# Kernel tuning notes

Hardware: AMD Instinct MI355X
Metric: run time of the kernel (lower is better)

Reference implementation:

```python
import jax, jax.numpy as jnp
import numpy as np

D = 32      # input_size
H = 256     # hidden_size
B = 4096    # batch
EPS = 1e-12

def _masks(order="A"):
    # Standard MADE degree-based masks. order 'A' = natural ordering.
    deg_in = np.arange(1, D + 1) if order == "A" else np.arange(D, 0, -1)
    deg_h = (np.arange(H) % (D - 1)) + 1
    m0 = (deg_h[None, :] >= deg_in[:, None]).astype(np.float32)  # [D,H] input->hidden
    m1 = (deg_h[None, :] >= deg_h[:, None]).astype(np.float32)   # [H,H] hidden->hidden
    m2 = (deg_in[None, :] > deg_h[:, None]).astype(np.float32)   # [H,D] hidden->output (strict)
    return jnp.asarray(m0), jnp.asarray(m1), jnp.asarray(m2)

M0, M1, M2 = _masks()

def _made(y, W0, b0, W1, b1, W2, b2):
    # masked MLP: D -> H -> H -> D (num_hiddens=2 hidden layers)
    h = jax.nn.relu(y @ (W0 * M0) + b0)
    h = jax.nn.relu(h @ (W1 * M1) + b1)
    return h @ (W2 * M2) + b2

def setup_inputs() -> dict:
    key = jax.random.key(0)
    ks = jax.random.split(key, 8)
    def w(k, fi, fo):
        return jax.random.normal(k, (fi, fo), jnp.float32) / np.sqrt(fi)
    inp = {"x": jax.random.normal(ks[0], (B, D), jnp.float32)}
    i = 1
    for n in ("mu", "lv"):
        inp[n + "_W0"] = w(ks[i], D, H); inp[n + "_b0"] = jnp.zeros((H,), jnp.float32); i += 1
        inp[n + "_W1"] = w(ks[i], H, H); inp[n + "_b1"] = jnp.zeros((H,), jnp.float32); i += 1
        inp[n + "_W2"] = w(ks[i], H, D); inp[n + "_b2"] = jnp.zeros((D,), jnp.float32); i += 1
    return inp

def reference(x, mu_W0, mu_b0, mu_W1, mu_b1, mu_W2, mu_b2,
              lv_W0, lv_b0, lv_W1, lv_b1, lv_W2, lv_b2):
    # AFMADEBlock.forward: D sequential fixed-point iterations of the
    def step(carry, _):
        y, _ls = carry
        mu = _made(y, mu_W0, mu_b0, mu_W1, mu_b1, mu_W2, mu_b2)
        logstd = _made(y, lv_W0, lv_b0, lv_W1, lv_b1, lv_W2, lv_b2) * 0.5
        y_new = (x - mu) / (jnp.exp(logstd) + EPS)
        return (y_new, logstd), None
    init = (jnp.zeros_like(x), jnp.zeros_like(x))
    (y, logstd), _ = jax.lax.scan(step, init, None, length=D)
    return y, logstd.sum(axis=1)
```

## Files before the change

### kernel.cpp

```cpp
#include <hip/hip_runtime.h>

#define DD   32
#define HH   256
#define BB   4096
#define RR   2
#define EPSF 1e-12f

__device__ __forceinline__ int made_pi(int p) {
    return (p < 72) ? (p / 9) + 31 * (p % 9)
                    : (8 + (p - 72) / 8) + 31 * ((p - 72) % 8);
}
__device__ __forceinline__ int made_off(int d) {
    return (d <= 9) ? 9 * (d - 1) : 8 * d;
}

#define NW0   (DD * HH)
#define NW1   (HH * HH)
#define NW2   (DD * HH)
#define NETF  (NW0 + NW1 + NW2 + HH + HH)
#define WSNEED ((size_t)(2 * NETF) * 4)

__global__ void made_prep(
    const float* __restrict__ muW0, const float* __restrict__ mub0,
    const float* __restrict__ muW1, const float* __restrict__ mub1,
    const float* __restrict__ muW2,
    const float* __restrict__ lvW0, const float* __restrict__ lvb0,
    const float* __restrict__ lvW1, const float* __restrict__ lvb1,
    const float* __restrict__ lvW2,
    float* __restrict__ ws)
{
    const int t = threadIdx.x;
    const int b = blockIdx.x;
    __shared__ float rowbuf[HH];

    if (b < 512) {
        const int n = b >> 8, p = b & 255;
        const int h = made_pi(p);
        const float* W1 = n ? lvW1 : muW1;
        float* o = ws + (size_t)n * NETF;
        *reinterpret_cast<float4*>(&rowbuf[4 * t]) =
            *reinterpret_cast<const float4*>(W1 + h * HH + 4 * t);
        __syncthreads();
        float4 w;
        w.x = rowbuf[made_pi(4 * t + 0)];
        w.y = rowbuf[made_pi(4 * t + 1)];
        w.z = rowbuf[made_pi(4 * t + 2)];
        w.w = rowbuf[made_pi(4 * t + 3)];
        *reinterpret_cast<float4*>(o + NW0 + p * HH + 4 * t) = w;
        if (t == 0) {
            o[NW0 + NW1 + NW2 + p]      = (n ? lvb0 : mub0)[h];
            o[NW0 + NW1 + NW2 + HH + p] = (n ? lvb1 : mub1)[h];
        }
    } else {
        const int idx   = b - 512;
        const int n     = idx >> 6;
        const int which = (idx >> 5) & 1;
        const int i     = idx & 31;
        float* o = ws + (size_t)n * NETF;
        if (which == 0) {
            const float* W0 = n ? lvW0 : muW0;
            *reinterpret_cast<float4*>(&rowbuf[4 * t]) =
                *reinterpret_cast<const float4*>(W0 + i * HH + 4 * t);
            __syncthreads();
            float4 w;
            w.x = rowbuf[made_pi(4 * t + 0)];
            w.y = rowbuf[made_pi(4 * t + 1)];
            w.z = rowbuf[made_pi(4 * t + 2)];
            w.w = rowbuf[made_pi(4 * t + 3)];
            *reinterpret_cast<float4*>(o + i * HH + 4 * t) = w;
        } else {
            const float* W2 = n ? lvW2 : muW2;
            float4 w;
            w.x = W2[made_pi(4 * t + 0) * DD + i];
            w.y = W2[made_pi(4 * t + 1) * DD + i];
            w.z = W2[made_pi(4 * t + 2) * DD + i];
            w.w = W2[made_pi(4 * t + 3) * DD + i];
            *reinterpret_cast<float4*>(o + NW0 + NW1 + i * HH + 4 * t) = w;
        }
    }
}

__global__ __launch_bounds__(256, 2) void made_main(
    const float* __restrict__ ws, const float* __restrict__ x,
    const float* __restrict__ mub2, const float* __restrict__ lvb2,
    float* __restrict__ out)
{
    const int lane = threadIdx.x & 63;
    const int wv   = threadIdx.x >> 6;
    const int row0 = ((blockIdx.x << 2) + wv) * RR;
    const int c4   = lane << 2;

    const float* W0p[2] = {ws,             ws + NETF};
    const float* W1p[2] = {ws + NW0,       ws + NETF + NW0};
    const float* W2p[2] = {ws + NW0 + NW1, ws + NETF + NW0 + NW1};

    float h0[2][4][RR], h1[2][4][RR], r1[2][4][RR];
    #pragma unroll
    for (int n = 0; n < 2; ++n) {
        const float* bb = ws + (size_t)n * NETF + NW0 + NW1 + NW2;
        const float4 v0 = *reinterpret_cast<const float4*>(bb + c4);
        const float4 v1 = *reinterpret_cast<const float4*>(bb + HH + c4);
        const float a0[4] = {v0.x, v0.y, v0.z, v0.w};
        const float a1[4] = {v1.x, v1.y, v1.z, v1.w};
        #pragma unroll
        for (int s = 0; s < 4; ++s)
            #pragma unroll
            for (int r = 0; r < RR; ++r) {
                h0[n][s][r] = a0[s];
                h1[n][s][r] = a1[s];
                r1[n][s][r] = 0.f;
            }
    }

    __shared__ float A[4][2][RR][12];

    float yprev[RR], lsum[RR], ysave[RR];
    #pragma unroll
    for (int r = 0; r < RR; ++r) { yprev[r] = 0.f; lsum[r] = 0.f; ysave[r] = 0.f; }

    for (int d = 0; d < DD; ++d) {
        const int off  = (d >= 1) ? made_off(d) : 0;
        const int off2 = made_off(d + 1);
        const int nk   = off2 - off;

        if (d >= 1) {
            const int ls = off >> 2;
            if (lane >= ls) {
                #pragma unroll
                for (int n = 0; n < 2; ++n) {
                    const float4 w = *reinterpret_cast<const float4*>(
                        W0p[n] + (d - 1) * HH + c4);
                    #pragma unroll
                    for (int r = 0; r < RR; ++r) {
                        h0[n][0][r] = fmaf(yprev[r], w.x, h0[n][0][r]);
                        h0[n][1][r] = fmaf(yprev[r], w.y, h0[n][1][r]);
                        h0[n][2][r] = fmaf(yprev[r], w.z, h0[n][2][r]);
                        h0[n][3][r] = fmaf(yprev[r], w.w, h0[n][3][r]);
                    }
                }
            }
            #pragma unroll
            for (int s = 0; s < 4; ++s) {
                const int p = c4 + s;
                if (p >= off && p < off2) {
                    const int k = p - off;
                    #pragma unroll
                    for (int r = 0; r < RR; ++r) {
                        A[wv][0][r][k] = fmaxf(h0[0][s][r], 0.f);
                        A[wv][1][r][k] = fmaxf(h0[1][s][r], 0.f);
                    }
                }
            }
            float av[2][RR][9];
            #pragma unroll
            for (int n = 0; n < 2; ++n)
                #pragma unroll
                for (int r = 0; r < RR; ++r) {
                    const float4 a03 = *reinterpret_cast<const float4*>(&A[wv][n][r][0]);
                    const float4 a47 = *reinterpret_cast<const float4*>(&A[wv][n][r][4]);
                    av[n][r][0] = a03.x; av[n][r][1] = a03.y;
                    av[n][r][2] = a03.z; av[n][r][3] = a03.w;
                    av[n][r][4] = a47.x; av[n][r][5] = a47.y;
                    av[n][r][6] = a47.z; av[n][r][7] = a47.w;
                    av[n][r][8] = A[wv][n][r][8];
                }

            if (lane >= ls) {
                #pragma unroll
                for (int n = 0; n < 2; ++n) {
                    const float* W1r = W1p[n] + off * HH + c4;
                    #pragma unroll
                    for (int k = 0; k < 8; ++k) {
                        const float4 w = *reinterpret_cast<const float4*>(W1r + k * HH);
                        #pragma unroll
                        for (int r = 0; r < RR; ++r) {
                            h1[n][0][r] = fmaf(av[n][r][k], w.x, h1[n][0][r]);
                            h1[n][1][r] = fmaf(av[n][r][k], w.y, h1[n][1][r]);
                            h1[n][2][r] = fmaf(av[n][r][k], w.z, h1[n][2][r]);
                            h1[n][3][r] = fmaf(av[n][r][k], w.w, h1[n][3][r]);
                        }
                    }
                }
                if (nk == 9) {
                    #pragma unroll
                    for (int n = 0; n < 2; ++n) {
                        const float4 w = *reinterpret_cast<const float4*>(
                            W1p[n] + (off + 8) * HH + c4);
                        #pragma unroll
                        for (int r = 0; r < RR; ++r) {
                            h1[n][0][r] = fmaf(av[n][r][8], w.x, h1[n][0][r]);
                            h1[n][1][r] = fmaf(av[n][r][8], w.y, h1[n][1][r]);
                            h1[n][2][r] = fmaf(av[n][r][8], w.z, h1[n][2][r]);
                            h1[n][3][r] = fmaf(av[n][r][8], w.w, h1[n][3][r]);
                        }
                    }
                }
            }
            #pragma unroll
            for (int s = 0; s < 4; ++s) {
                const int p = c4 + s;
                if (p >= off && p < off2) {
                    #pragma unroll
                    for (int r = 0; r < RR; ++r) {
                        r1[0][s][r] = fmaxf(h1[0][s][r], 0.f);
                        r1[1][s][r] = fmaxf(h1[1][s][r], 0.f);
                    }
                }
            }
        }

        float red[2][RR];
        #pragma unroll
        for (int n = 0; n < 2; ++n)
            #pragma unroll
            for (int r = 0; r < RR; ++r) red[n][r] = 0.f;
        if (c4 < off2) {
            #pragma unroll
            for (int n = 0; n < 2; ++n) {
                const float4 w = *reinterpret_cast<const float4*>(W2p[n] + d * HH + c4);
                #pragma unroll
                for (int r = 0; r < RR; ++r)
                    red[n][r] = fmaf(r1[n][0][r], w.x, fmaf(r1[n][1][r], w.y,
                                fmaf(r1[n][2][r], w.z, r1[n][3][r] * w.w)));
            }
        }
        #pragma unroll
        for (int m = 1; m < 64; m <<= 1)
            #pragma unroll
            for (int n = 0; n < 2; ++n)
                #pragma unroll
                for (int r = 0; r < RR; ++r)
                    red[n][r] += __shfl_xor(red[n][r], m, 64);

        const float b2m = mub2[d];
        const float b2l = lvb2[d];
        #pragma unroll
        for (int r = 0; r < RR; ++r) {
            const float mu  = red[0][r] + b2m;
            const float ls2 = 0.5f * (red[1][r] + b2l);
            lsum[r] += ls2;
            const float yd = (x[(row0 + r) * DD + d] - mu) / (__expf(ls2) + EPSF);
            yprev[r] = yd;
            if (lane == d) ysave[r] = yd;
        }
    }

    #pragma unroll
    for (int r = 0; r < RR; ++r) {
        if (lane < DD) out[(row0 + r) * DD + lane] = ysave[r];
        if (lane == 0) out[BB * DD + row0 + r] = lsum[r];
    }
}

__global__ __launch_bounds__(64, 1) void made_inv_fb(
    const float* __restrict__ x,
    const float* __restrict__ muW0, const float* __restrict__ mub0,
    const float* __restrict__ muW1, const float* __restrict__ mub1,
    const float* __restrict__ muW2, const float* __restrict__ mub2,
    const float* __restrict__ lvW0, const float* __restrict__ lvb0,
    const float* __restrict__ lvW1, const float* __restrict__ lvb1,
    const float* __restrict__ lvW2, const float* __restrict__ lvb2,
    float* __restrict__ out)
{
    const int lane    = threadIdx.x;
    const int rowBase = blockIdx.x * 4;
    const int hb      = lane << 2;
    int deg[4];
    #pragma unroll
    for (int s = 0; s < 4; ++s) deg[s] = ((hb + s) % 31) + 1;
    const float* Wp0[2] = {muW0, lvW0};
    const float* Bp0[2] = {mub0, lvb0};
    const float* Wp1[2] = {muW1, lvW1};
    const float* Bp1[2] = {mub1, lvb1};
    const float* Wp2[2] = {muW2, lvW2};
    float h0pre[2][4][4], h1pre[2][4][4], r1[2][4][4], yprev[4], lsum[4];
    #pragma unroll
    for (int n = 0; n < 2; ++n) {
        const float4 b0v = *reinterpret_cast<const float4*>(Bp0[n] + hb);
        const float4 b1v = *reinterpret_cast<const float4*>(Bp1[n] + hb);
        const float b0a[4] = {b0v.x, b0v.y, b0v.z, b0v.w};
        const float b1a[4] = {b1v.x, b1v.y, b1v.z, b1v.w};
        #pragma unroll
        for (int s = 0; s < 4; ++s)
            #pragma unroll
            for (int r = 0; r < 4; ++r) {
                h0pre[n][s][r] = b0a[s]; h1pre[n][s][r] = b1a[s]; r1[n][s][r] = 0.f;
            }
    }
    #pragma unroll
    for (int r = 0; r < 4; ++r) { yprev[r] = 0.f; lsum[r] = 0.f; }
    __shared__ float lds_a[2][4][12];
    for (int d = 0; d < DD; ++d) {
        if (d >= 1) {
            #pragma unroll
            for (int n = 0; n < 2; ++n) {
                const float4 w0 = *reinterpret_cast<const float4*>(Wp0[n] + (d - 1) * HH + hb);
                const float w0a[4] = {w0.x, w0.y, w0.z, w0.w};
                #pragma unroll
                for (int s = 0; s < 4; ++s)
                    #pragma unroll
                    for (int r = 0; r < 4; ++r)
                        h0pre[n][s][r] = fmaf(yprev[r], w0a[s], h0pre[n][s][r]);
            }
            #pragma unroll
            for (int n = 0; n < 2; ++n)
                #pragma unroll
                for (int s = 0; s < 4; ++s)
                    if (deg[s] == d) {
                        const int k = (hb + s - (d - 1)) / 31;
                        #pragma unroll
                        for (int r = 0; r < 4; ++r)
                            lds_a[n][r][k] = fmaxf(h0pre[n][s][r], 0.f);
                    }
            __syncthreads();
            const bool nine = (d <= 8);
            #pragma unroll
            for (int n = 0; n < 2; ++n) {
                const float* W1r = Wp1[n] + (size_t)(d - 1) * HH + hb;
                float4 w1v[9];
                #pragma unroll
                for (int k = 0; k < 8; ++k)
                    w1v[k] = *reinterpret_cast<const float4*>(W1r + k * 31 * HH);
                if (nine) w1v[8] = *reinterpret_cast<const float4*>(W1r + 8 * 31 * HH);
                #pragma unroll
                for (int r = 0; r < 4; ++r) {
                    const float4 a03 = *reinterpret_cast<const float4*>(&lds_a[n][r][0]);
                    const float4 a47 = *reinterpret_cast<const float4*>(&lds_a[n][r][4]);
                    const float av[8] = {a03.x, a03.y, a03.z, a03.w, a47.x, a47.y, a47.z, a47.w};
                    #pragma unroll
                    for (int k = 0; k < 8; ++k) {
                        const float wk[4] = {w1v[k].x, w1v[k].y, w1v[k].z, w1v[k].w};
                        #pragma unroll
                        for (int s = 0; s < 4; ++s)
                            h1pre[n][s][r] = fmaf(av[k], wk[s], h1pre[n][s][r]);
                    }
                    if (nine) {
                        const float a8 = lds_a[n][r][8];
                        const float wk[4] = {w1v[8].x, w1v[8].y, w1v[8].z, w1v[8].w};
                        #pragma unroll
                        for (int s = 0; s < 4; ++s)
                            h1pre[n][s][r] = fmaf(a8, wk[s], h1pre[n][s][r]);
                    }
                }
            }
            #pragma unroll
            for (int n = 0; n < 2; ++n)
                #pragma unroll
                for (int s = 0; s < 4; ++s)
                    if (deg[s] == d)
                        #pragma unroll
                        for (int r = 0; r < 4; ++r)
                            r1[n][s][r] = fmaxf(h1pre[n][s][r], 0.f);
            __syncthreads();
        }
        float w2v[2][4];
        #pragma unroll
        for (int n = 0; n < 2; ++n)
            #pragma unroll
            for (int s = 0; s < 4; ++s)
                w2v[n][s] = Wp2[n][(hb + s) * DD + d];
        float red[2][4];
        #pragma unroll
        for (int n = 0; n < 2; ++n)
            #pragma unroll
            for (int r = 0; r < 4; ++r) {
                float p = 0.f;
                #pragma unroll
                for (int s = 0; s < 4; ++s) p = fmaf(r1[n][s][r], w2v[n][s], p);
                red[n][r] = p;
            }
        #pragma unroll
        for (int m = 1; m < 64; m <<= 1)
            #pragma unroll
            for (int n = 0; n < 2; ++n)
                #pragma unroll
                for (int r = 0; r < 4; ++r)
                    red[n][r] += __shfl_xor(red[n][r], m, 64);
        const float b2m = mub2[d], b2l = lvb2[d];
        #pragma unroll
        for (int r = 0; r < 4; ++r) {
            const float mu = red[0][r] + b2m;
            const float logstd = 0.5f * (red[1][r] + b2l);
            lsum[r] += logstd;
            const float yd = (x[(rowBase + r) * DD + d] - mu) / (__expf(logstd) + EPSF);
            yprev[r] = yd;
            if (lane == 0) out[(rowBase + r) * DD + d] = yd;
        }
    }
    if (lane == 0)
        #pragma unroll
        for (int r = 0; r < 4; ++r) out[BB * DD + rowBase + r] = lsum[r];
}

extern "C" void kernel_launch(void* const* d_in, const int* in_sizes, int n_in,
                              void* d_out, int out_size, void* d_ws, size_t ws_size,
                              hipStream_t stream) {
    const float* x    = (const float*)d_in[0];
    const float* muW0 = (const float*)d_in[1];
    const float* mub0 = (const float*)d_in[2];
    const float* muW1 = (const float*)d_in[3];
    const float* mub1 = (const float*)d_in[4];
    const float* muW2 = (const float*)d_in[5];
    const float* mub2 = (const float*)d_in[6];
    const float* lvW0 = (const float*)d_in[7];
    const float* lvb0 = (const float*)d_in[8];
    const float* lvW1 = (const float*)d_in[9];
    const float* lvb1 = (const float*)d_in[10];
    const float* lvW2 = (const float*)d_in[11];
    const float* lvb2 = (const float*)d_in[12];
    float* out = (float*)d_out;

    if (ws_size >= WSNEED) {
        float* ws = (float*)d_ws;
        made_prep<<<dim3(640), dim3(64), 0, stream>>>(
            muW0, mub0, muW1, mub1, muW2,
            lvW0, lvb0, lvW1, lvb1, lvW2, ws);
        made_main<<<dim3(BB / (4 * RR)), dim3(256), 0, stream>>>(ws, x, mub2, lvb2, out);
    } else {
        made_inv_fb<<<dim3(BB / 4), dim3(64), 0, stream>>>(x,
            muW0, mub0, muW1, mub1, muW2, mub2,
            lvW0, lvb0, lvW1, lvb1, lvW2, lvb2, out);
    }
}
```

Before: 163.3 us.

## Accumulate output layer incrementally per lane, replacing per-step wave reductions

The hidden-to-output layer is restructured so each lane owns one output (mu or logvar for one of 32 dims) and accumulates contributions from newly finalized hidden units each step via an interleaved W2 layout. This replaces the per-step dot product plus 6-level butterfly shuffle reduction with a few FMAs and two broadcast shuffles. x values are also preloaded into registers once, and the b2 bias is folded into the accumulator init. Finalized layer-2 activations now go through an extra LDS buffer, adding a shared-memory write and read per step.

```diff
diff --git a/kernel.cpp b/kernel.cpp
--- a/kernel.cpp
+++ b/kernel.cpp
@@ -16,9 +16,10 @@
 
 #define NW0   (DD * HH)
 #define NW1   (HH * HH)
-#define NW2   (DD * HH)
-#define NETF  (NW0 + NW1 + NW2 + HH + HH)
-#define WSNEED ((size_t)(2 * NETF) * 4)
+#define NETF  (NW0 + NW1 + HH + HH)
+#define W2IOFF (2 * NETF)
+#define NW2I  (HH * 64)
+#define WSNEED ((size_t)(W2IOFF + NW2I) * 4)
 
 __global__ void made_prep(
     const float* __restrict__ muW0, const float* __restrict__ mub0,
@@ -48,35 +49,28 @@
         w.w = rowbuf[made_pi(4 * t + 3)];
         *reinterpret_cast<float4*>(o + NW0 + p * HH + 4 * t) = w;
         if (t == 0) {
-            o[NW0 + NW1 + NW2 + p]      = (n ? lvb0 : mub0)[h];
-            o[NW0 + NW1 + NW2 + HH + p] = (n ? lvb1 : mub1)[h];
+            o[NW0 + NW1 + p]      = (n ? lvb0 : mub0)[h];
+            o[NW0 + NW1 + HH + p] = (n ? lvb1 : mub1)[h];
         }
+    } else if (b < 768) {
+        const int p = b - 512;
+        const int h = made_pi(p);
+        const int n = t >> 5, dd = t & 31;
+        ws[W2IOFF + p * 64 + t] = (n ? lvW2 : muW2)[h * DD + dd];
     } else {
-        const int idx   = b - 512;
-        const int n     = idx >> 6;
-        const int which = (idx >> 5) & 1;
-        const int i     = idx & 31;
+        const int idx = b - 768;
+        const int n = idx >> 5, i = idx & 31;
+        const float* W0 = n ? lvW0 : muW0;
         float* o = ws + (size_t)n * NETF;
-        if (which == 0) {
-            const float* W0 = n ? lvW0 : muW0;
-            *reinterpret_cast<float4*>(&rowbuf[4 * t]) =
-                *reinterpret_cast<const float4*>(W0 + i * HH + 4 * t);
-            __syncthreads();
-            float4 w;
-            w.x = rowbuf[made_pi(4 * t + 0)];
-            w.y = rowbuf[made_pi(4 * t + 1)];
-            w.z = rowbuf[made_pi(4 * t + 2)];
-            w.w = rowbuf[made_pi(4 * t + 3)];
-            *reinterpret_cast<float4*>(o + i * HH + 4 * t) = w;
-        } else {
-            const float* W2 = n ? lvW2 : muW2;
-            float4 w;
-            w.x = W2[made_pi(4 * t + 0) * DD + i];
-            w.y = W2[made_pi(4 * t + 1) * DD + i];
-            w.z = W2[made_pi(4 * t + 2) * DD + i];
-            w.w = W2[made_pi(4 * t + 3) * DD + i];
-            *reinterpret_cast<float4*>(o + NW0 + NW1 + i * HH + 4 * t) = w;
-        }
+        *reinterpret_cast<float4*>(&rowbuf[4 * t]) =
+            *reinterpret_cast<const float4*>(W0 + i * HH + 4 * t);
+        __syncthreads();
+        float4 w;
+        w.x = rowbuf[made_pi(4 * t + 0)];
+        w.y = rowbuf[made_pi(4 * t + 1)];
+        w.z = rowbuf[made_pi(4 * t + 2)];
+        w.w = rowbuf[made_pi(4 * t + 3)];
+        *reinterpret_cast<float4*>(o + i * HH + 4 * t) = w;
     }
 }
 
@@ -89,15 +83,17 @@
     const int wv   = threadIdx.x >> 6;
     const int row0 = ((blockIdx.x << 2) + wv) * RR;
     const int c4   = lane << 2;
-
-    const float* W0p[2] = {ws,             ws + NETF};
-    const float* W1p[2] = {ws + NW0,       ws + NETF + NW0};
-    const float* W2p[2] = {ws + NW0 + NW1, ws + NETF + NW0 + NW1};
-
-    float h0[2][4][RR], h1[2][4][RR], r1[2][4][RR];
+    const int nn   = lane >> 5;
+    const int ddl  = lane & 31;
+
+    const float* W0p[2] = {ws,       ws + NETF};
+    const float* W1p[2] = {ws + NW0, ws + NETF + NW0};
+    const float* W2i    = ws + W2IOFF;
+
+    float h0[2][4][RR], h1[2][4][RR];
     #pragma unroll
     for (int n = 0; n < 2; ++n) {
-        const float* bb = ws + (size_t)n * NETF + NW0 + NW1 + NW2;
+        const float* bb = ws + (size_t)n * NETF + NW0 + NW1;
         const float4 v0 = *reinterpret_cast<const float4*>(bb + c4);
         const float4 v1 = *reinterpret_cast<const float4*>(bb + HH + c4);
         const float a0[4] = {v0.x, v0.y, v0.z, v0.w};
@@ -105,26 +101,32 @@
         #pragma unroll
         for (int s = 0; s < 4; ++s)
             #pragma unroll
-            for (int r = 0; r < RR; ++r) {
-                h0[n][s][r] = a0[s];
-                h1[n][s][r] = a1[s];
-                r1[n][s][r] = 0.f;
-            }
-    }
+            for (int r = 0; r < RR; ++r) { h0[n][s][r] = a0[s]; h1[n][s][r] = a1[s]; }
+    }
+
+    const float accinit = nn ? lvb2[ddl] : mub2[ddl];
+    float acc[RR];
+    #pragma unroll
+    for (int r = 0; r < RR; ++r) acc[r] = accinit;
+
+    float xvr[RR];
+    #pragma unroll
+    for (int r = 0; r < RR; ++r) xvr[r] = x[(row0 + r) * DD + ddl];
 
     __shared__ float A[4][2][RR][12];
+    __shared__ float Bf[4][2][RR][12];
 
     float yprev[RR], lsum[RR], ysave[RR];
     #pragma unroll
     for (int r = 0; r < RR; ++r) { yprev[r] = 0.f; lsum[r] = 0.f; ysave[r] = 0.f; }
 
     for (int d = 0; d < DD; ++d) {
-        const int off  = (d >= 1) ? made_off(d) : 0;
-        const int off2 = made_off(d + 1);
-        const int nk   = off2 - off;
-
         if (d >= 1) {
-            const int ls = off >> 2;
+            const int off  = made_off(d);
+            const int off2 = made_off(d + 1);
+            const int nk   = off2 - off;
+            const int ls   = off >> 2;
+
             if (lane >= ls) {
                 #pragma unroll
                 for (int n = 0; n < 2; ++n) {
@@ -141,9 +143,8 @@
             }
             #pragma unroll
             for (int s = 0; s < 4; ++s) {
-                const int p = c4 + s;
-                if (p >= off && p < off2) {
-                    const int k = p - off;
+                const int k = c4 + s - off;
+                if ((unsigned)k < (unsigned)nk) {
                     #pragma unroll
                     for (int r = 0; r < RR; ++r) {
                         A[wv][0][r][k] = fmaxf(h0[0][s][r], 0.f);
@@ -181,7 +182,7 @@
                         }
                     }
                 }
-                if (nk == 9) {
+                if (d <= 8) {
                     #pragma unroll
                     for (int n = 0; n < 2; ++n) {
                         const float4 w = *reinterpret_cast<const float4*>(
@@ -198,48 +199,47 @@
             }
             #pragma unroll
             for (int s = 0; s < 4; ++s) {
-                const int p = c4 + s;
-                if (p >= off && p < off2) {
+                const int k = c4 + s - off;
+                if ((unsigned)k < (unsigned)nk) {
                     #pragma unroll
                     for (int r = 0; r < RR; ++r) {
-                        r1[0][s][r] = fmaxf(h1[0][s][r], 0.f);
-                        r1[1][s][r] = fmaxf(h1[1][s][r], 0.f);
-                    }
-                }
+                        Bf[wv][0][r][k] = fmaxf(h1[0][s][r], 0.f);
+                        Bf[wv][1][r][k] = fmaxf(h1[1][s][r], 0.f);
+                    }
+                }
+            }
+            float rb[RR][9];
+            #pragma unroll
+            for (int r = 0; r < RR; ++r) {
+                const float4 b03 = *reinterpret_cast<const float4*>(&Bf[wv][nn][r][0]);
+                const float4 b47 = *reinterpret_cast<const float4*>(&Bf[wv][nn][r][4]);
+                rb[r][0] = b03.x; rb[r][1] = b03.y; rb[r][2] = b03.z; rb[r][3] = b03.w;
+                rb[r][4] = b47.x; rb[r][5] = b47.y; rb[r][6] = b47.z; rb[r][7] = b47.w;
+                rb[r][8] = Bf[wv][nn][r][8];
+            }
+            const float* w2c = W2i + off * 64 + lane;
+            #pragma unroll
+            for (int k = 0; k < 8; ++k) {
+                const float w2 = w2c[k * 64];
+                #pragma unroll
+                for (int r = 0; r < RR; ++r)
+                    acc[r] = fmaf(rb[r][k], w2, acc[r]);
+            }
+            if (d <= 8) {
+                const float w2 = w2c[8 * 64];
+                #pragma unroll
+                for (int r = 0; r < RR; ++r)
+                    acc[r] = fmaf(rb[r][8], w2, acc[r]);
             }
         }
 
-        float red[2][RR];
-        #pragma unroll
-        for (int n = 0; n < 2; ++n)
-            #pragma unroll
-            for (int r = 0; r < RR; ++r) red[n][r] = 0.f;
-        if (c4 < off2) {
-            #pragma unroll
-            for (int n = 0; n < 2; ++n) {
-                const float4 w = *reinterpret_cast<const float4*>(W2p[n] + d * HH + c4);
-                #pragma unroll
-                for (int r = 0; r < RR; ++r)
-                    red[n][r] = fmaf(r1[n][0][r], w.x, fmaf(r1[n][1][r], w.y,
-                                fmaf(r1[n][2][r], w.z, r1[n][3][r] * w.w)));
-            }
-        }
-        #pragma unroll
-        for (int m = 1; m < 64; m <<= 1)
-            #pragma unroll
-            for (int n = 0; n < 2; ++n)
-                #pragma unroll
-                for (int r = 0; r < RR; ++r)
-                    red[n][r] += __shfl_xor(red[n][r], m, 64);
-
-        const float b2m = mub2[d];
-        const float b2l = lvb2[d];
         #pragma unroll
         for (int r = 0; r < RR; ++r) {
-            const float mu  = red[0][r] + b2m;
-            const float ls2 = 0.5f * (red[1][r] + b2l);
+            const float mu  = __shfl(acc[r], d, 64);
+            const float lv  = __shfl(acc[r], 32 + d, 64);
+            const float ls2 = 0.5f * lv;
             lsum[r] += ls2;
-            const float yd = (x[(row0 + r) * DD + d] - mu) / (__expf(ls2) + EPSF);
+            const float yd = (__shfl(xvr[r], d, 64) - mu) / (__expf(ls2) + EPSF);
             yprev[r] = yd;
             if (lane == d) ysave[r] = yd;
         }
@@ -412,7 +412,7 @@
 
     if (ws_size >= WSNEED) {
         float* ws = (float*)d_ws;
-        made_prep<<<dim3(640), dim3(64), 0, stream>>>(
+        made_prep<<<dim3(832), dim3(64), 0, stream>>>(
             muW0, mub0, muW1, mub1, muW2,
             lvW0, lvb0, lvW1, lvb1, lvW2, ws);
         made_main<<<dim3(BB / (4 * RR)), dim3(256), 0, stream>>>(ws, x, mub2, lvb2, out);
```

New measurement: 151.0 us. 7.6% less time.
